# Performance work log

Hardware: AMD Instinct MI355X
Metric: run time of the kernel (lower is better)

## Reference

```python
import jax, jax.numpy as jnp
import numpy as np

N = 4096      # nodes
E = 131072    # edges (before self loops)
C = 512       # channels
H = 8         # heads
CO = C // H   # per-head out channels (64)
EPS = 1e-5
NEG_SLOPE = 0.2


def layer_norm(x, g, b):
    mu = jnp.mean(x, axis=-1, keepdims=True)
    var = jnp.mean((x - mu) ** 2, axis=-1, keepdims=True)
    return (x - mu) * jax.lax.rsqrt(var + EPS) * g + b


def gatv2(x, src, dst, wl, bl, wr, br, att, bias):
    # PyG GATv2Conv, concat=True, add_self_loops handled by caller.
    n = x.shape[0]
    xl = (x @ wl.T + bl).reshape(n, H, CO)   # target-side features
    xr = (x @ wr.T + br).reshape(n, H, CO)   # source-side features (messages)
    e = jax.nn.leaky_relu(xl[dst] + xr[src], NEG_SLOPE)   # [E+N, H, CO]
    alpha = jnp.einsum('ehc,hc->eh', e, att)              # [E+N, H]
    # segment softmax over destination neighborhoods
    amax = jax.ops.segment_max(alpha, dst, num_segments=n)
    ex = jnp.exp(alpha - amax[dst])
    denom = jax.ops.segment_sum(ex, dst, num_segments=n)
    a = ex / denom[dst]                                   # [E+N, H]
    msg = xr[src] * a[:, :, None]                         # [E+N, H, CO]
    out = jax.ops.segment_sum(msg, dst, num_segments=n)   # [N, H, CO]
    return out.reshape(n, H * CO) + bias


def mha(x, in_w, in_b, out_w, out_b):
    # nn.MultiheadAttention self-attention, batch=1, eval mode
    n = x.shape[0]
    qkv = x @ in_w.T + in_b                               # [N, 3C]
    q, k, v = jnp.split(qkv, 3, axis=-1)
    q = q.reshape(n, H, CO); k = k.reshape(n, H, CO); v = v.reshape(n, H, CO)
    scores = jnp.einsum('qhd,khd->hqk', q, k) / jnp.sqrt(jnp.float32(CO))
    p = jax.nn.softmax(scores, axis=-1)
    o = jnp.einsum('hqk,khd->qhd', p, v).reshape(n, C)
    return o @ out_w.T + out_b


def setup_inputs() -> dict:
    key = jax.random.key(0)
    ks = jax.random.split(key, 24)
    s = 0.02
    d = {}
    d['x'] = jax.random.normal(ks[0], (N, C), jnp.float32)
    d['edge_index'] = jax.random.randint(ks[1], (2, E), 0, N, dtype=jnp.int64)
    d['gat_wl'] = jax.random.normal(ks[2], (H * CO, C), jnp.float32) * s
    d['gat_bl'] = jnp.zeros((H * CO,), jnp.float32)
    d['gat_wr'] = jax.random.normal(ks[3], (H * CO, C), jnp.float32) * s
    d['gat_br'] = jnp.zeros((H * CO,), jnp.float32)
    d['gat_att'] = jax.random.normal(ks[4], (H, CO), jnp.float32) * s
    d['gat_b'] = jnp.zeros((H * CO,), jnp.float32)
    d['in_w'] = jax.random.normal(ks[5], (3 * C, C), jnp.float32) * s
    d['in_b'] = jnp.zeros((3 * C,), jnp.float32)
    d['out_w'] = jax.random.normal(ks[6], (C, C), jnp.float32) * s
    d['out_b'] = jnp.zeros((C,), jnp.float32)
    d['ln1_g'] = jnp.ones((C,), jnp.float32); d['ln1_b'] = jnp.zeros((C,), jnp.float32)
    d['ln2_g'] = jnp.ones((C,), jnp.float32); d['ln2_b'] = jnp.zeros((C,), jnp.float32)
    d['ln3_g'] = jnp.ones((C,), jnp.float32); d['ln3_b'] = jnp.zeros((C,), jnp.float32)
    d['w1'] = jax.random.normal(ks[7], (4 * C, C), jnp.float32) * s
    d['b1'] = jnp.zeros((4 * C,), jnp.float32)
    d['w2'] = jax.random.normal(ks[8], (C, 4 * C), jnp.float32) * s
    d['b2'] = jnp.zeros((C,), jnp.float32)
    return d


def reference(x, edge_index, gat_wl, gat_bl, gat_wr, gat_br, gat_att, gat_b,
              in_w, in_b, out_w, out_b, ln1_g, ln1_b, ln2_g, ln2_b,
              ln3_g, ln3_b, w1, b1, w2, b2):
    n = x.shape[0]
    loops = jnp.arange(n, dtype=edge_index.dtype)
    src = jnp.concatenate([edge_index[0], loops])
    dst = jnp.concatenate([edge_index[1], loops])
    h_local = gatv2(x, src, dst, gat_wl, gat_bl, gat_wr, gat_br, gat_att, gat_b)
    x = layer_norm(x + h_local, ln1_g, ln1_b)
    h_global = mha(x, in_w, in_b, out_w, out_b)
    x = layer_norm(x + h_global, ln2_g, ln2_b)
    h_ffn = (jax.nn.gelu(x @ w1.T + b1, approximate=False)) @ w2.T + b2
    x = layer_norm(x + h_ffn, ln3_g, ln3_b)
    return x
```

## Files before the change

### kernel.cpp

```cpp
#include <hip/hip_runtime.h>
#include <math.h>

#define NN 4096
#define CC 512
#define EE 131072
#define NEDGE (EE + NN)
#define HH 8
#define DCO 64
#define NC2 2097152L

typedef __attribute__((ext_vector_type(8))) short bfrag;
typedef __attribute__((ext_vector_type(4))) float f32x4;
typedef __attribute__((ext_vector_type(4))) int i32x4;

__device__ __forceinline__ float bf2f(unsigned short u) {
  union { float f; unsigned int i; } x; x.i = ((unsigned int)u) << 16; return x.f;
}
__device__ __forceinline__ unsigned short f2bf(float f) {
  union { float f; unsigned int i; } x; x.f = f;
  unsigned int r = x.i + 0x7FFFu + ((x.i >> 16) & 1u);
  return (unsigned short)(r >> 16);
}
__device__ __forceinline__ unsigned short f2bf_trunc(float f) {
  union { float f; unsigned int i; } x; x.f = f;
  return (unsigned short)(x.i >> 16);
}

__device__ __forceinline__ void gld16(const unsigned short* g, unsigned short* l) {
  __builtin_amdgcn_global_load_lds(
      (__attribute__((address_space(1))) unsigned int*)g,
      (__attribute__((address_space(3))) unsigned int*)l, 16, 0, 0);
}

#define QSC 0.18033688011112042f

#define CX  2097152L
#define CWL (CX + 262144L)
#define CWR (CWL + 262144L)
#define CIW (CWR + 786432L)
#define COW (CIW + 262144L)
#define CW1 (COW + 1048576L)
#define CW2 (CW1 + 1048576L)

__global__ void cvt_all(const float* __restrict__ x, const float* __restrict__ wl,
                        const float* __restrict__ wr, const float* __restrict__ iw,
                        const float* __restrict__ ow, const float* __restrict__ w1,
                        const float* __restrict__ w2, unsigned short* __restrict__ dst,
                        int* __restrict__ cntcur, const float* __restrict__ bl,
                        const float* __restrict__ br, float* __restrict__ biasc) {
  if (blockIdx.x >= 5632) {
    int t = threadIdx.x;
    if (blockIdx.x == 5632) {
      for (int k = t; k < 8192; k += 256) cntcur[k] = 0;
    } else {
      for (int k = t; k < 512; k += 256) {
        biasc[k] = bl[k];
        biasc[512 + k] = br[k];
      }
    }
    return;
  }
  long i = ((long)blockIdx.x * 256 + threadIdx.x) * 4;
  const float* s; long o;
  if (i < CX)       { s = x;  o = i; }
  else if (i < CWL) { s = wl; o = i - CX; }
  else if (i < CWR) { s = wr; o = i - CWL; }
  else if (i < CIW) { s = iw; o = i - CWR; }
  else if (i < COW) { s = ow; o = i - CIW; }
  else if (i < CW1) { s = w1; o = i - COW; }
  else              { s = w2; o = i - CW1; }
  f32x4 v = *(const f32x4*)(s + o);
  union { unsigned long long q; unsigned short u[4]; } t;
#pragma unroll
  for (int j = 0; j < 4; j++) t.u[j] = f2bf(v[j]);
  *(unsigned long long*)(dst + i) = t.q;
}

template<int OMODE, int TN, bool SPLIT>
__global__ __launch_bounds__(256) void gemm_t(
    const unsigned short* __restrict__ A, const unsigned short* __restrict__ B,
    const float* __restrict__ bias, void* __restrict__ C,
    int K, int lda, int ldb, int ldc)
{
  __shared__ unsigned short As[4096];
  __shared__ unsigned short Bs[TN * 32];
  constexpr int MI = (TN == 128) ? 4 : 2;
  const int tid = threadIdx.x;
  const int wave = tid >> 6, lane = tid & 63;
  const int ml = lane & 15, kq = lane >> 4;
  const int wm = (TN == 128) ? ((wave >> 1) << 6) : (wave << 5);
  const int wn = (TN == 128) ? ((wave & 1) << 6) : 0;
  const int bm = blockIdx.y << 7, bn = blockIdx.x * TN;
  const int srow = tid >> 2, scol = (tid & 3) << 3;
  if (SPLIT) { A += (long)blockIdx.z * K; B += (long)blockIdx.z * K; }
  const float* biasp = (!SPLIT || blockIdx.z == 0) ? bias : nullptr;
  const unsigned short* Ag = A + (long)(bm + srow) * lda + scol;
  const unsigned short* Bg = B + (long)(bn + srow) * ldb + scol;
  const long astep = (long)64 * lda, bstep = (long)64 * ldb;
  unsigned short* lA0 = As + tid * 8;
  unsigned short* lA1 = As + 2048 + tid * 8;
  unsigned short* lB0 = Bs + tid * 8;
  f32x4 acc[MI][4];
#pragma unroll
  for (int mi = 0; mi < MI; mi++)
#pragma unroll
    for (int ni = 0; ni < 4; ni++) acc[mi][ni] = (f32x4){0.f, 0.f, 0.f, 0.f};
  for (int k0 = 0; k0 < K; k0 += 32) {
    __syncthreads();
    gld16(Ag, lA0); gld16(Ag + astep, lA1);
    gld16(Bg, lB0);
    if (TN == 128) gld16(Bg + bstep, Bs + 2048 + tid * 8);
    Ag += 32; Bg += 32;
    __syncthreads();
    bfrag af[MI], bf[4];
#pragma unroll
    for (int mi = 0; mi < MI; mi++)
      af[mi] = *(const bfrag*)&As[(wm + (mi << 4) + ml) * 32 + (kq << 3)];
#pragma unroll
    for (int ni = 0; ni < 4; ni++)
      bf[ni] = *(const bfrag*)&Bs[(wn + (ni << 4) + ml) * 32 + (kq << 3)];
#pragma unroll
    for (int mi = 0; mi < MI; mi++)
#pragma unroll
      for (int ni = 0; ni < 4; ni++)
        acc[mi][ni] = __builtin_amdgcn_mfma_f32_16x16x32_bf16(af[mi], bf[ni], acc[mi][ni], 0, 0, 0);
  }
#pragma unroll
  for (int ni = 0; ni < 4; ni++) {
    int col = bn + wn + (ni << 4) + ml;
    float bb = biasp ? biasp[col] : 0.f;
#pragma unroll
    for (int mi = 0; mi < MI; mi++) {
      int row0 = bm + wm + (mi << 4) + (kq << 2);
#pragma unroll
      for (int r = 0; r < 4; r++) {
        float v = acc[mi][ni][r] + bb;
        int row = row0 + r;
        if (OMODE == 3) {
          unsigned short* q = (unsigned short*)C;
          if (col < 512) {
            int h = col >> 6, d = col & 63;
            q[(long)h * (NN * DCO) + (long)row * DCO + d] = f2bf(v * QSC);
          } else if (col < 1024) {
            int c2 = col - 512, h = c2 >> 6, d = c2 & 63;
            q[NC2 + (long)h * (NN * DCO) + (long)row * DCO + d] = f2bf(v);
          } else {
            int c2 = col - 1024, h = c2 >> 6, d = c2 & 63;
            q[2 * NC2 + (long)h * (DCO * NN) + (long)d * NN + row] = f2bf(v);
          }
        } else if (OMODE == 0) {
          long off = (SPLIT ? (long)blockIdx.z * NC2 : 0) + (long)row * ldc + col;
          ((float*)C)[off] = v;
        } else {
          if (OMODE == 2) v = 0.5f * v * (1.f + erff(v * 0.70710678118f));
          ((unsigned short*)C)[(long)row * ldc + col] = f2bf(v);
        }
      }
    }
  }
}

__global__ void count_k(const int* __restrict__ ei, int* __restrict__ cnt) {
  int e = blockIdx.x * 256 + threadIdx.x;
  if (e >= NEDGE) return;
  int d = (e < EE) ? ei[EE + e] : (e - EE);
  atomicAdd(&cnt[d], 1);
}

__global__ void scan_k(const int* __restrict__ cnt, int* __restrict__ rowptr) {
  __shared__ int s[1024];
  int t = threadIdx.x;
  int b = t * 4;
  int c0 = cnt[b], c1 = cnt[b + 1], c2 = cnt[b + 2], c3 = cnt[b + 3];
  int sum = c0 + c1 + c2 + c3;
  s[t] = sum;
  __syncthreads();
  for (int o = 1; o < 1024; o <<= 1) {
    int v = (t >= o) ? s[t - o] : 0;
    __syncthreads();
    s[t] += v;
    __syncthreads();
  }
  int ex = s[t] - sum;
  rowptr[b] = ex; rowptr[b + 1] = ex + c0;
  rowptr[b + 2] = ex + c0 + c1; rowptr[b + 3] = ex + c0 + c1 + c2;
  if (t == 1023) rowptr[4096] = ex + sum;
}

__global__ void scatter_k(const int* __restrict__ ei, const int* __restrict__ rowptr,
                          int* __restrict__ cur, int* __restrict__ order) {
  int e = blockIdx.x * 256 + threadIdx.x;
  if (e >= NEDGE) return;
  int d = (e < EE) ? ei[EE + e] : (e - EE);
  int p = atomicAdd(&cur[d], 1);
  order[rowptr[d] + p] = e;
}

__global__ __launch_bounds__(256) void gat_alpha(
    const unsigned short* __restrict__ xlr, const int* __restrict__ order,
    const int* __restrict__ ei, const float* __restrict__ att,
    float* __restrict__ alpha)
{
  int i = (blockIdx.x << 2) + (threadIdx.x >> 6);
  int e = order[i];
  int lane = threadIdx.x & 63;
  int src, dst;
  if (e < EE) { src = ei[e]; dst = ei[EE + e]; } else { src = dst = e - EE; }
  int c = lane << 3;
  union { i32x4 v; unsigned short u[8]; } L, R;
  L.v = *(const i32x4*)(xlr + (long)dst * 1024 + c);
  R.v = *(const i32x4*)(xlr + (long)src * 1024 + 512 + c);
  f32x4 t0 = *(const f32x4*)(att + c);
  f32x4 t1 = *(const f32x4*)(att + c + 4);
  float p = 0.f;
#pragma unroll
  for (int j = 0; j < 8; j++) {
    float x = bf2f(L.u[j]) + bf2f(R.u[j]);
    x = (x > 0.f) ? x : 0.2f * x;
    float tv = (j < 4) ? t0[j] : t1[j - 4];
    p += tv * x;
  }
  p += __shfl_xor(p, 1); p += __shfl_xor(p, 2); p += __shfl_xor(p, 4);
  if ((lane & 7) == 0) alpha[(long)i * 8 + (lane >> 3)] = __expf(p);
}

__global__ __launch_bounds__(256) void gat_aggr(
    const unsigned short* __restrict__ xlr, const float* __restrict__ alpha,
    const int* __restrict__ order, const int* __restrict__ rowptr,
    const int* __restrict__ ei, const float* __restrict__ gbias,
    float* __restrict__ out)
{
  __shared__ float red[256];
  __shared__ float sinv[8];
  __shared__ float part[4][512];
  int n = blockIdx.x, t = threadIdx.x;
  int beg = rowptr[n], deg = rowptr[n + 1] - beg;
  int h8 = t & 7, grp = t >> 3;
  float s = 0.f;
  for (int i = grp; i < deg; i += 32)
    s += alpha[(long)(beg + i) * 8 + h8];
  red[t] = s; __syncthreads();
  for (int off = 128; off >= 8; off >>= 1) {
    if (t < off) red[t] += red[t + off];
    __syncthreads();
  }
  if (t < 8) sinv[t] = 1.f / red[t];
  __syncthreads();
  int wave = t >> 6, lane = t & 63;
  int ch = lane << 3;
  int hh = lane >> 3;
  float acc[8];
#pragma unroll
  for (int j = 0; j < 8; j++) acc[j] = 0.f;
  for (int i = wave; i < deg; i += 4) {
    int e = order[beg + i];
    int sn = (e < EE) ? ei[e] : (e - EE);
    float wgt = alpha[(long)(beg + i) * 8 + hh];
    union { i32x4 v; unsigned short u[8]; } X;
    X.v = *(const i32x4*)(xlr + (long)sn * 1024 + 512 + ch);
#pragma unroll
    for (int j = 0; j < 8; j++) acc[j] += wgt * bf2f(X.u[j]);
  }
  *(f32x4*)&part[wave][ch]     = (f32x4){acc[0], acc[1], acc[2], acc[3]};
  *(f32x4*)&part[wave][ch + 4] = (f32x4){acc[4], acc[5], acc[6], acc[7]};
  __syncthreads();
#pragma unroll
  for (int c = t; c < 512; c += 256) {
    float v = part[0][c] + part[1][c] + part[2][c] + part[3][c];
    out[(long)n * CC + c] = v * sinv[c >> 6] + gbias[c];
  }
}

template<int NS>
__global__ __launch_bounds__(256) void resid_ln(
    const float* __restrict__ a, const float* __restrict__ b,
    const float* __restrict__ g, const float* __restrict__ be,
    float* __restrict__ of, unsigned short* __restrict__ ob)
{
  __shared__ float sh[8];
  int row = blockIdx.x, t = threadIdx.x;
  long base = (long)row * CC;
  float b0 = 0.f, b1 = 0.f;
#pragma unroll
  for (int s = 0; s < NS; s++) {
    b0 += b[(long)s * NC2 + base + t];
    b1 += b[(long)s * NC2 + base + t + 256];
  }
  float v0 = a[base + t] + b0;
  float v1 = a[base + t + 256] + b1;
  float s = v0 + v1, ss = v0 * v0 + v1 * v1;
  for (int o = 32; o > 0; o >>= 1) { s += __shfl_down(s, o); ss += __shfl_down(ss, o); }
  int wave = t >> 6, lane = t & 63;
  if (lane == 0) { sh[wave] = s; sh[4 + wave] = ss; }
  __syncthreads();
  float S = sh[0] + sh[1] + sh[2] + sh[3];
  float SS = sh[4] + sh[5] + sh[6] + sh[7];
  float mean = S * (1.f / 512.f);
  float var = SS * (1.f / 512.f) - mean * mean;
  float rs = rsqrtf(var + 1e-5f);
  float y0 = (v0 - mean) * rs * g[t] + be[t];
  float y1 = (v1 - mean) * rs * g[t + 256] + be[t + 256];
  if (of) { of[base + t] = y0; of[base + t + 256] = y1; }
  if (ob) { ob[base + t] = f2bf(y0); ob[base + t + 256] = f2bf(y1); }
}

__global__ __launch_bounds__(256, 4) void flash_attn(
    const unsigned short* __restrict__ qkvP, unsigned short* __restrict__ Op,
    float* __restrict__ Lp)
{
  __shared__ unsigned short QP[128 * 72];
  __shared__ unsigned short Ks[64 * 72];
  __shared__ unsigned short Vs[64 * 72];
  const int tid = threadIdx.x;
  const int wave = tid >> 6, lane = tid & 63;
  const int ml = lane & 15, kq = lane >> 4;
  const int h = blockIdx.x & 7, qt = blockIdx.x >> 3;
  const int sp = blockIdx.y;
  const int n0 = qt << 7;
  const unsigned short* Qh = qkvP + (long)h * (NN * DCO);
  const unsigned short* Kh = qkvP + NC2 + (long)h * (NN * DCO);
  const unsigned short* Vh = qkvP + 2 * NC2 + (long)h * (DCO * NN);
  {
    int r = tid >> 1, c = (tid & 1) << 5;
    const unsigned short* src = Qh + (long)(n0 + r) * DCO + c;
    unsigned short* d = &QP[r * 72 + c];
    *(i32x4*)d        = *(const i32x4*)src;
    *(i32x4*)(d + 8)  = *(const i32x4*)(src + 8);
    *(i32x4*)(d + 16) = *(const i32x4*)(src + 16);
    *(i32x4*)(d + 24) = *(const i32x4*)(src + 24);
  }
  __syncthreads();
  bfrag aq[2][2];
#pragma unroll
  for (int s = 0; s < 2; s++)
#pragma unroll
    for (int kh = 0; kh < 2; kh++)
      aq[s][kh] = *(const bfrag*)&QP[(wave * 32 + s * 16 + ml) * 72 + kh * 32 + (kq << 3)];
  bfrag ones;
#pragma unroll
  for (int j = 0; j < 8; j++) ones[j] = (short)0x3F80;
  f32x4 Oa[2][4];
  f32x4 Lc[2];
#pragma unroll
  for (int s = 0; s < 2; s++) {
    Lc[s] = (f32x4){0.f, 0.f, 0.f, 0.f};
#pragma unroll
    for (int dg = 0; dg < 4; dg++) Oa[s][dg] = (f32x4){0.f, 0.f, 0.f, 0.f};
  }
  const int r_ = tid >> 2, c_ = (tid & 3) << 4;
  const int j0 = sp << 4;
  i32x4 ka, kb, va, vb;
  {
    int k0 = j0 << 6;
    ka = *(const i32x4*)(Kh + (long)(k0 + r_) * DCO + c_);
    kb = *(const i32x4*)(Kh + (long)(k0 + r_) * DCO + c_ + 8);
    va = *(const i32x4*)(Vh + (long)r_ * NN + k0 + c_);
    vb = *(const i32x4*)(Vh + (long)r_ * NN + k0 + c_ + 8);
  }
  for (int jj = 0; jj < 16; jj++) {
    if (jj) __syncthreads();
    *(i32x4*)&Ks[r_ * 72 + c_] = ka; *(i32x4*)&Ks[r_ * 72 + c_ + 8] = kb;
    *(i32x4*)&Vs[r_ * 72 + c_] = va; *(i32x4*)&Vs[r_ * 72 + c_ + 8] = vb;
    __syncthreads();
    if (jj < 15) {
      int k0 = (j0 + jj + 1) << 6;
      ka = *(const i32x4*)(Kh + (long)(k0 + r_) * DCO + c_);
      kb = *(const i32x4*)(Kh + (long)(k0 + r_) * DCO + c_ + 8);
      va = *(const i32x4*)(Vh + (long)r_ * NN + k0 + c_);
      vb = *(const i32x4*)(Vh + (long)r_ * NN + k0 + c_ + 8);
    }
    f32x4 sc[2][4];
#pragma unroll
    for (int s = 0; s < 2; s++)
#pragma unroll
      for (int c = 0; c < 4; c++) sc[s][c] = (f32x4){0.f, 0.f, 0.f, 0.f};
#pragma unroll
    for (int c = 0; c < 4; c++) {
      bfrag bk0 = *(const bfrag*)&Ks[(c * 16 + ml) * 72 + (kq << 3)];
      bfrag bk1 = *(const bfrag*)&Ks[(c * 16 + ml) * 72 + 32 + (kq << 3)];
#pragma unroll
      for (int s = 0; s < 2; s++) {
        sc[s][c] = __builtin_amdgcn_mfma_f32_16x16x32_bf16(aq[s][0], bk0, sc[s][c], 0, 0, 0);
        sc[s][c] = __builtin_amdgcn_mfma_f32_16x16x32_bf16(aq[s][1], bk1, sc[s][c], 0, 0, 0);
      }
    }
#pragma unroll
    for (int s = 0; s < 2; s++)
#pragma unroll
      for (int c = 0; c < 4; c++)
#pragma unroll
        for (int r = 0; r < 4; r++) {
          float p = exp2f(sc[s][c][r]);
          QP[(wave * 32 + s * 16 + (kq << 2) + r) * 72 + c * 16 + ml] = f2bf_trunc(p);
        }
    bfrag ap[2][2];
#pragma unroll
    for (int s = 0; s < 2; s++)
#pragma unroll
      for (int kh = 0; kh < 2; kh++)
        ap[s][kh] = *(const bfrag*)&QP[(wave * 32 + s * 16 + ml) * 72 + kh * 32 + (kq << 3)];
#pragma unroll
    for (int s = 0; s < 2; s++) {
      Lc[s] = __builtin_amdgcn_mfma_f32_16x16x32_bf16(ap[s][0], ones, Lc[s], 0, 0, 0);
      Lc[s] = __builtin_amdgcn_mfma_f32_16x16x32_bf16(ap[s][1], ones, Lc[s], 0, 0, 0);
    }
#pragma unroll
    for (int dg = 0; dg < 4; dg++) {
      bfrag bv0 = *(const bfrag*)&Vs[(dg * 16 + ml) * 72 + (kq << 3)];
      bfrag bv1 = *(const bfrag*)&Vs[(dg * 16 + ml) * 72 + 32 + (kq << 3)];
#pragma unroll
      for (int s = 0; s < 2; s++) {
        Oa[s][dg] = __builtin_amdgcn_mfma_f32_16x16x32_bf16(ap[s][0], bv0, Oa[s][dg], 0, 0, 0);
        Oa[s][dg] = __builtin_amdgcn_mfma_f32_16x16x32_bf16(ap[s][1], bv1, Oa[s][dg], 0, 0, 0);
      }
    }
  }
  long obase = (long)sp * NC2;
#pragma unroll
  for (int s = 0; s < 2; s++)
#pragma unroll
    for (int dg = 0; dg < 4; dg++)
#pragma unroll
      for (int r = 0; r < 4; r++) {
        int row = wave * 32 + s * 16 + (kq << 2) + r;
        Op[obase + (long)(n0 + row) * CC + (h << 6) + (dg << 4) + ml] = f2bf(Oa[s][dg][r]);
      }
  if (ml == 0) {
#pragma unroll
    for (int s = 0; s < 2; s++)
#pragma unroll
      for (int r = 0; r < 4; r++) {
        int row = wave * 32 + s * 16 + (kq << 2) + r;
        Lp[(long)sp * (NN * HH) + (long)(n0 + row) * HH + h] = Lc[s][r];
      }
  }
}

__global__ void flash_combine(const unsigned short* __restrict__ Op,
                              const float* __restrict__ Lp,
                              unsigned short* __restrict__ Ao) {
  int idx = blockIdx.x * 256 + threadIdx.x;
  int n = idx >> 9, c = idx & 511, h = c >> 6;
  float l = 0.f, o = 0.f;
#pragma unroll
  for (int s = 0; s < 4; s++) {
    l += Lp[(long)s * (NN * HH) + (long)n * HH + h];
    o += bf2f(Op[(long)s * NC2 + idx]);
  }
  Ao[idx] = f2bf(o / l);
}

extern "C" void kernel_launch(void* const* d_in, const int* in_sizes, int n_in,
                              void* d_out, int out_size, void* d_ws, size_t ws_size,
                              hipStream_t stream) {
  typedef unsigned short u16;
  const float* x      = (const float*)d_in[0];
  const int*   ei     = (const int*)d_in[1];
  const float* wl     = (const float*)d_in[2];
  const float* bl     = (const float*)d_in[3];
  const float* wr     = (const float*)d_in[4];
  const float* br     = (const float*)d_in[5];
  const float* att    = (const float*)d_in[6];
  const float* gat_b  = (const float*)d_in[7];
  const float* in_w   = (const float*)d_in[8];
  const float* in_b   = (const float*)d_in[9];
  const float* out_w  = (const float*)d_in[10];
  const float* out_b  = (const float*)d_in[11];
  const float* ln1g   = (const float*)d_in[12];
  const float* ln1b   = (const float*)d_in[13];
  const float* ln2g   = (const float*)d_in[14];
  const float* ln2b   = (const float*)d_in[15];
  const float* ln3g   = (const float*)d_in[16];
  const float* ln3b   = (const float*)d_in[17];
  const float* w1     = (const float*)d_in[18];
  const float* b1     = (const float*)d_in[19];
  const float* w2     = (const float*)d_in[20];
  const float* b2     = (const float*)d_in[21];

  const size_t MB = 1u << 20;
  char* w = (char*)d_ws;
  float* h_f32   = (float*)(w + 0);
  float* x2_f32  = (float*)(w + 8 * MB);
  int*   cnt     = (int*)(w + 16 * MB);
  int*   cur     = cnt + 4096;
  int*   rowptr  = (int*)(w + 16 * MB + 32 * 1024);
  int*   order   = (int*)(w + 16 * MB + 64 * 1024);
  u16*   cvt     = (u16*)(w + 17 * MB);
  u16*   xbf     = cvt;
  u16*   wlrbf   = cvt + CX;
  u16*   inwbf   = cvt + CWR;
  u16*   outwbf  = cvt + CIW;
  u16*   w1bf    = cvt + COW;
  u16*   w2bf    = cvt + CW1;
  u16*   xlr_bf  = (u16*)(w + 29 * MB);
  float* alpha   = (float*)(w + 37 * MB);
  float* gat_out = (float*)(w + 42 * MB);
  u16*   Opart   = (u16*)(w + 29 * MB);
  float* proj    = (float*)(w + 29 * MB);
  u16*   ffn1    = (u16*)(w + 61 * MB);
  u16*   qkvP    = (u16*)(w + 93 * MB);
  float* biasc   = (float*)(w + 105 * MB);
  float* Lpart   = (float*)(w + 105 * MB);
  u16*   Ao      = (u16*)(w + 106 * MB);
  u16*   actb    = (u16*)(w + 110 * MB);

  cvt_all<<<5634, 256, 0, stream>>>(x, wl, wr, in_w, out_w, w1, w2, cvt,
                                    cnt, bl, br, biasc);
  count_k<<<(NEDGE + 255) / 256, 256, 0, stream>>>(ei, cnt);
  scan_k<<<1, 1024, 0, stream>>>(cnt, rowptr);
  scatter_k<<<(NEDGE + 255) / 256, 256, 0, stream>>>(ei, rowptr, cur, order);

  gemm_t<1, 64, false><<<dim3(16, 32), 256, 0, stream>>>(xbf, wlrbf, biasc, xlr_bf, 512, 512, 512, 1024);
  gat_alpha<<<NEDGE / 4, 256, 0, stream>>>(xlr_bf, order, ei, att, alpha);
  gat_aggr<<<NN, 256, 0, stream>>>(xlr_bf, alpha, order, rowptr, ei, gat_b, gat_out);
  resid_ln<1><<<NN, 256, 0, stream>>>(x, gat_out, ln1g, ln1b, h_f32, actb);

  gemm_t<3, 64, false><<<dim3(24, 32), 256, 0, stream>>>(actb, inwbf, in_b, qkvP, 512, 512, 512, 0);
  flash_attn<<<dim3(256, 4), 256, 0, stream>>>(qkvP, Opart, Lpart);
  flash_combine<<<(NN * CC) / 256, 256, 0, stream>>>(Opart, Lpart, Ao);
  gemm_t<0, 64, true><<<dim3(8, 32, 2), 256, 0, stream>>>(Ao, outwbf, out_b, proj, 256, 512, 512, 512);
  resid_ln<2><<<NN, 256, 0, stream>>>(h_f32, proj, ln2g, ln2b, x2_f32, actb);

  gemm_t<2, 128, false><<<dim3(16, 32), 256, 0, stream>>>(actb, w1bf, b1, ffn1, 512, 512, 512, 2048);
  gemm_t<0, 128, true><<<dim3(4, 32, 4), 256, 0, stream>>>(ffn1, w2bf, b2, proj, 512, 2048, 2048, 512);
  resid_ln<4><<<NN, 256, 0, stream>>>(x2_f32, proj, ln3g, ln3b, (float*)d_out, nullptr);
}
```

Baseline: 368.0 us.

## Fuse GAT attention scores, aggregation and residual LayerNorm into one kernel

```diff
diff --git a/kernel.cpp b/kernel.cpp
--- a/kernel.cpp
+++ b/kernel.cpp
@@ -196,79 +196,96 @@
   order[rowptr[d] + p] = e;
 }
 
-__global__ __launch_bounds__(256) void gat_alpha(
-    const unsigned short* __restrict__ xlr, const int* __restrict__ order,
+__global__ __launch_bounds__(256) void gat_fused(
+    const unsigned short* __restrict__ xlr, const float* __restrict__ x,
+    const int* __restrict__ order, const int* __restrict__ rowptr,
     const int* __restrict__ ei, const float* __restrict__ att,
-    float* __restrict__ alpha)
+    const float* __restrict__ gbias,
+    const float* __restrict__ g, const float* __restrict__ be,
+    float* __restrict__ of, unsigned short* __restrict__ ob)
 {
-  int i = (blockIdx.x << 2) + (threadIdx.x >> 6);
-  int e = order[i];
-  int lane = threadIdx.x & 63;
-  int src, dst;
-  if (e < EE) { src = ei[e]; dst = ei[EE + e]; } else { src = dst = e - EE; }
-  int c = lane << 3;
-  union { i32x4 v; unsigned short u[8]; } L, R;
-  L.v = *(const i32x4*)(xlr + (long)dst * 1024 + c);
-  R.v = *(const i32x4*)(xlr + (long)src * 1024 + 512 + c);
-  f32x4 t0 = *(const f32x4*)(att + c);
-  f32x4 t1 = *(const f32x4*)(att + c + 4);
-  float p = 0.f;
-#pragma unroll
-  for (int j = 0; j < 8; j++) {
-    float x = bf2f(L.u[j]) + bf2f(R.u[j]);
-    x = (x > 0.f) ? x : 0.2f * x;
-    float tv = (j < 4) ? t0[j] : t1[j - 4];
-    p += tv * x;
-  }
-  p += __shfl_xor(p, 1); p += __shfl_xor(p, 2); p += __shfl_xor(p, 4);
-  if ((lane & 7) == 0) alpha[(long)i * 8 + (lane >> 3)] = __expf(p);
-}
-
-__global__ __launch_bounds__(256) void gat_aggr(
-    const unsigned short* __restrict__ xlr, const float* __restrict__ alpha,
-    const int* __restrict__ order, const int* __restrict__ rowptr,
-    const int* __restrict__ ei, const float* __restrict__ gbias,
-    float* __restrict__ out)
-{
-  __shared__ float red[256];
+  __shared__ float part[4][512];
+  __shared__ float sw[4][8];
   __shared__ float sinv[8];
-  __shared__ float part[4][512];
+  __shared__ float shl[8];
   int n = blockIdx.x, t = threadIdx.x;
   int beg = rowptr[n], deg = rowptr[n + 1] - beg;
-  int h8 = t & 7, grp = t >> 3;
-  float s = 0.f;
-  for (int i = grp; i < deg; i += 32)
-    s += alpha[(long)(beg + i) * 8 + h8];
-  red[t] = s; __syncthreads();
-  for (int off = 128; off >= 8; off >>= 1) {
-    if (t < off) red[t] += red[t + off];
-    __syncthreads();
-  }
-  if (t < 8) sinv[t] = 1.f / red[t];
-  __syncthreads();
   int wave = t >> 6, lane = t & 63;
   int ch = lane << 3;
-  int hh = lane >> 3;
+  union U8 { i32x4 v; unsigned short u[8]; };
+  U8 XL; XL.v = *(const i32x4*)(xlr + (long)n * 1024 + ch);
+  float xl[8];
+#pragma unroll
+  for (int j = 0; j < 8; j++) xl[j] = bf2f(XL.u[j]);
+  f32x4 t0 = *(const f32x4*)(att + ch);
+  f32x4 t1 = *(const f32x4*)(att + ch + 4);
   float acc[8];
 #pragma unroll
   for (int j = 0; j < 8; j++) acc[j] = 0.f;
-  for (int i = wave; i < deg; i += 4) {
+  float se = 0.f;
+  int i = wave;
+  U8 X;
+  if (i < deg) {
     int e = order[beg + i];
     int sn = (e < EE) ? ei[e] : (e - EE);
-    float wgt = alpha[(long)(beg + i) * 8 + hh];
-    union { i32x4 v; unsigned short u[8]; } X;
     X.v = *(const i32x4*)(xlr + (long)sn * 1024 + 512 + ch);
-#pragma unroll
-    for (int j = 0; j < 8; j++) acc[j] += wgt * bf2f(X.u[j]);
+  }
+  while (i < deg) {
+    U8 Xc = X;
+    int inext = i + 4;
+    if (inext < deg) {
+      int e = order[beg + inext];
+      int sn = (e < EE) ? ei[e] : (e - EE);
+      X.v = *(const i32x4*)(xlr + (long)sn * 1024 + 512 + ch);
+    }
+    float xr[8];
+    float p = 0.f;
+#pragma unroll
+    for (int j = 0; j < 8; j++) {
+      xr[j] = bf2f(Xc.u[j]);
+      float v = xl[j] + xr[j];
+      v = (v > 0.f) ? v : 0.2f * v;
+      float tv = (j < 4) ? t0[j] : t1[j - 4];
+      p += tv * v;
+    }
+    p += __shfl_xor(p, 1); p += __shfl_xor(p, 2); p += __shfl_xor(p, 4);
+    float ew = __expf(p);
+    se += ew;
+#pragma unroll
+    for (int j = 0; j < 8; j++) acc[j] += ew * xr[j];
+    i = inext;
   }
   *(f32x4*)&part[wave][ch]     = (f32x4){acc[0], acc[1], acc[2], acc[3]};
   *(f32x4*)&part[wave][ch + 4] = (f32x4){acc[4], acc[5], acc[6], acc[7]};
+  if ((lane & 7) == 0) sw[wave][lane >> 3] = se;
   __syncthreads();
-#pragma unroll
-  for (int c = t; c < 512; c += 256) {
-    float v = part[0][c] + part[1][c] + part[2][c] + part[3][c];
-    out[(long)n * CC + c] = v * sinv[c >> 6] + gbias[c];
-  }
+  if (t < 8) sinv[t] = 1.f / (sw[0][t] + sw[1][t] + sw[2][t] + sw[3][t]);
+  __syncthreads();
+  long base = (long)n * CC;
+  float v0, v1;
+  {
+    int c = t;
+    float p4 = part[0][c] + part[1][c] + part[2][c] + part[3][c];
+    v0 = x[base + c] + p4 * sinv[c >> 6] + gbias[c];
+  }
+  {
+    int c = t + 256;
+    float p4 = part[0][c] + part[1][c] + part[2][c] + part[3][c];
+    v1 = x[base + c] + p4 * sinv[c >> 6] + gbias[c];
+  }
+  float s = v0 + v1, ss = v0 * v0 + v1 * v1;
+  for (int o = 32; o > 0; o >>= 1) { s += __shfl_down(s, o); ss += __shfl_down(ss, o); }
+  if (lane == 0) { shl[wave] = s; shl[4 + wave] = ss; }
+  __syncthreads();
+  float S = shl[0] + shl[1] + shl[2] + shl[3];
+  float SS = shl[4] + shl[5] + shl[6] + shl[7];
+  float mean = S * (1.f / 512.f);
+  float var = SS * (1.f / 512.f) - mean * mean;
+  float rs = rsqrtf(var + 1e-5f);
+  float y0 = (v0 - mean) * rs * g[t] + be[t];
+  float y1 = (v1 - mean) * rs * g[t + 256] + be[t + 256];
+  of[base + t] = y0; of[base + t + 256] = y1;
+  ob[base + t] = f2bf(y0); ob[base + t + 256] = f2bf(y1);
 }
 
 template<int NS>
@@ -493,8 +510,6 @@
   u16*   w1bf    = cvt + COW;
   u16*   w2bf    = cvt + CW1;
   u16*   xlr_bf  = (u16*)(w + 29 * MB);
-  float* alpha   = (float*)(w + 37 * MB);
-  float* gat_out = (float*)(w + 42 * MB);
   u16*   Opart   = (u16*)(w + 29 * MB);
   float* proj    = (float*)(w + 29 * MB);
   u16*   ffn1    = (u16*)(w + 61 * MB);
@@ -511,9 +526,8 @@
   scatter_k<<<(NEDGE + 255) / 256, 256, 0, stream>>>(ei, rowptr, cur, order);
 
   gemm_t<1, 64, false><<<dim3(16, 32), 256, 0, stream>>>(xbf, wlrbf, biasc, xlr_bf, 512, 512, 512, 1024);
-  gat_alpha<<<NEDGE / 4, 256, 0, stream>>>(xlr_bf, order, ei, att, alpha);
-  gat_aggr<<<NN, 256, 0, stream>>>(xlr_bf, alpha, order, rowptr, ei, gat_b, gat_out);
-  resid_ln<1><<<NN, 256, 0, stream>>>(x, gat_out, ln1g, ln1b, h_f32, actb);
+  gat_fused<<<NN, 256, 0, stream>>>(xlr_bf, x, order, rowptr, ei, att, gat_b,
+                                    ln1g, ln1b, h_f32, actb);
 
   gemm_t<3, 64, false><<<dim3(24, 32), 256, 0, stream>>>(actb, inwbf, in_b, qkvP, 512, 512, 512, 0);
   flash_attn<<<dim3(256, 4), 256, 0, stream>>>(qkvP, Opart, Lpart);
```

New measurement: 323.9 us. 1.14x faster.
